# Kernel tuning notes

Hardware: AMD Instinct MI355X
Metric: run time of the kernel (lower is better)

Reference implementation:

```python
import jax, jax.numpy as jnp
import numpy as np

H, D = 20, 64  # heads, head_dim (hidden_size = 1280)


def setup_inputs() -> dict:
    key = jax.random.key(0)
    ks = jax.random.split(key, 10)
    B, S, HID, CROSS, T_TXT, T_IP = 8, 4096, 1280, 2048, 77, 4
    w = lambda k, shp: jax.random.normal(k, shp, dtype=jnp.float32) * 0.02
    return {
        "hidden_states": jax.random.normal(ks[0], (B, S, HID), dtype=jnp.float32),
        "encoder_hidden_states": jax.random.normal(ks[1], (B, T_TXT, CROSS), dtype=jnp.float32),
        "ip_hidden_states": jax.random.normal(ks[2], (B, T_IP, CROSS), dtype=jnp.float32),
        "Wq": w(ks[3], (HID, HID)),
        "Wk": w(ks[4], (CROSS, HID)),
        "Wv": w(ks[5], (CROSS, HID)),
        "Wk_ip": w(ks[6], (CROSS, HID)),
        "Wv_ip": w(ks[7], (CROSS, HID)),
        "Wo": w(ks[8], (HID, HID)),
        "bo": jnp.zeros((HID,), dtype=jnp.float32),
    }


def _attend(q, kv_in, Wk, Wv):
    # q: [B,S,H,D]; kv_in: [B,T,cross]
    B, T = kv_in.shape[0], kv_in.shape[1]
    k = (kv_in @ Wk).reshape(B, T, H, D)
    v = (kv_in @ Wv).reshape(B, T, H, D)
    scale = 1.0 / jnp.sqrt(jnp.asarray(D, q.dtype))
    scores = jnp.einsum("bqhd,bkhd->bhqk", q, k) * scale
    probs = jax.nn.softmax(scores, axis=-1)
    out = jnp.einsum("bhqk,bkhd->bqhd", probs, v)
    return out.reshape(B, q.shape[1], H * D)


def reference(hidden_states, encoder_hidden_states, ip_hidden_states,
              Wq, Wk, Wv, Wk_ip, Wv_ip, Wo, bo):
    B, S, _ = hidden_states.shape
    q = (hidden_states @ Wq).reshape(B, S, H, D)
    # text cross-attention branch
    out = _attend(q, encoder_hidden_states, Wk, Wv)
    # IP-adapter branch (single adapter, scale=1.0, no mask)
    ip_scale = 1.0
    out = out + ip_scale * _attend(q, ip_hidden_states, Wk_ip, Wv_ip)
    # output projection (dropout is identity at inference)
    return out @ Wo + bo
```

## Files before the change

kernel.cpp:

```cpp
#include <hip/hip_runtime.h>

using u16 = unsigned short;
using u32 = unsigned int;
typedef __bf16 bf16x8 __attribute__((ext_vector_type(8)));
typedef float f32x4 __attribute__((ext_vector_type(4)));
typedef float f32x16 __attribute__((ext_vector_type(16)));

__device__ __forceinline__ u16 f2bf(float f) {
  u32 u = __float_as_uint(f);
  u += 0x7FFFu + ((u >> 16) & 1u);
  return (u16)(u >> 16);
}

__device__ __forceinline__ u32 cvtpk(float a, float b) {
  u32 r;
  asm("v_cvt_pk_bf16_f32 %0, %1, %2" : "=v"(r) : "v"(a), "v"(b));
  return r;
}

__device__ __forceinline__ void gload16(const u16* g, u16* l) {
  __builtin_amdgcn_global_load_lds((const __attribute__((address_space(1))) void*)g,
                                   (__attribute__((address_space(3))) void*)l, 16, 0, 0);
}

__global__ void prep_all(const float* __restrict__ enc, const float* __restrict__ ip,
                         u16* __restrict__ a_all,
                         const float* __restrict__ Wk, const float* __restrict__ Wv,
                         const float* __restrict__ Wkip, const float* __restrict__ Wvip,
                         u16* __restrict__ kvw,
                         const float* __restrict__ Wq, const float* __restrict__ Wo,
                         u16* __restrict__ wq_t, u16* __restrict__ wo_t) {
  const int bid = blockIdx.x;
  const int tid = threadIdx.x;
  if (bid < 1536) {
    const int i = bid * 256 + tid;
    const int row = i >> 9;
    const int c4 = i & 511;
    ushort4 o = {0, 0, 0, 0};
    const float4* src = nullptr;
    if (row < 616) src = (const float4*)enc + (size_t)row * 512 + c4;
    else if (row >= 640 && row < 672) src = (const float4*)ip + (size_t)(row - 640) * 512 + c4;
    if (src) {
      const float4 v = *src;
      o.x = f2bf(v.x); o.y = f2bf(v.y); o.z = f2bf(v.z); o.w = f2bf(v.w);
    }
    ((ushort4*)a_all)[i] = o;
    return;
  }
  __shared__ float tile[32][33];
  const int x = tid & 31, y = tid >> 5;
  const float* in;
  u16* out;
  int K, N, n0, k0;
  if (bid < 11776) {
    const int f = bid - 1536;
    const int z = f / 2560, rem = f % 2560;
    in = (z == 0) ? Wk : (z == 1) ? Wv : (z == 2) ? Wkip : Wvip;
    out = kvw + (size_t)z * 1280 * 2048;
    K = 2048; N = 1280;
    n0 = (rem % 40) << 5; k0 = (rem / 40) << 5;
  } else {
    const int f = bid - 11776;
    const int z = f / 1600, rem = f % 1600;
    in = z ? Wo : Wq;
    out = z ? wo_t : wq_t;
    K = 1280; N = 1280;
    n0 = (rem % 40) << 5; k0 = (rem / 40) << 5;
  }
#pragma unroll
  for (int i = 0; i < 32; i += 8)
    tile[y + i][x] = in[(size_t)(k0 + y + i) * N + n0 + x];
  __syncthreads();
#pragma unroll
  for (int i = 0; i < 32; i += 8)
    out[(size_t)(n0 + y + i) * K + k0 + x] = f2bf(tile[x][y + i]);
}

#define MFMA16(a, b, c) __builtin_amdgcn_mfma_f32_16x16x32_bf16(a, b, c, 0, 0, 0)
#define MFMA32(a, b, c) __builtin_amdgcn_mfma_f32_32x32x16_bf16(a, b, c, 0, 0, 0)

template <int MODE, int CONV>
__global__ __launch_bounds__(512, 2) void gemm256(
    const u16* __restrict__ A, const u16* __restrict__ Bt,
    u16* __restrict__ Cb, const u16* __restrict__ kvcP, const u16* __restrict__ vtP,
    const float* __restrict__ convSrc, u16* __restrict__ convDst,
    int M, int N, int K) {
  const int tid = threadIdx.x;

  if (CONV) {
    if (blockIdx.x >= 60) {
      const float4* src = (const float4*)convSrc;
      ushort4* dst = (ushort4*)convDst;
      const long base = (long)(blockIdx.x - 60) * 4096 + tid;
#pragma unroll
      for (int k = 0; k < 8; ++k) {
        const float4 v = src[base + k * 512];
        ushort4 o;
        o.x = f2bf(v.x); o.y = f2bf(v.y); o.z = f2bf(v.z); o.w = f2bf(v.w);
        dst[base + k * 512] = o;
      }
      return;
    }
  }

  __shared__ __align__(16) u16 smem[67584];
  u16* As = smem;
  u16* Bs = smem + 32768;

  const int w = tid >> 6, lane = tid & 63;
  const int lo = lane & 15, hi = lane >> 4;
  const int wm = w >> 2, wn = w & 3;

  const int nbn = N >> 8;
  int wg = blockIdx.x;
  if (!CONV) {
    const int nwg = gridDim.x;
    const int q = nwg >> 3, r = nwg & 7;
    const int xcd = wg & 7, l = wg >> 3;
    wg = (xcd < r ? xcd * (q + 1) : r * (q + 1) + (xcd - r) * q) + l;
  }
  const int bm = wg / nbn, bn = wg % nbn;
  const int m0 = bm << 8, n0 = bn << 8;
  const int NT = K >> 6;

  const int sr = lane >> 3;
  const int sc8 = ((lane & 7) ^ sr) << 3;
  const u16* pA[2];
  const u16* pB[2];
#pragma unroll
  for (int i = 0; i < 2; ++i) {
    const int rr = (i * 8 + w) * 8 + sr;
    pA[i] = A + (size_t)(m0 + rr) * K + sc8;
    pB[i] = Bt + (size_t)(n0 + rr) * K + sc8;
  }
  const int ch0 = w * 512, ch1 = (8 + w) * 512;

#define STAGE_A(h, tt)                                                     \
  {                                                                        \
    const int ttc = ((tt) < NT) ? (tt) : (NT - 1);                         \
    u16* d = As + ((((tt)&1) * 2 + (h)) << 13);                            \
    const size_t off = (size_t)(h)*128 * K + (size_t)ttc * 64;             \
    gload16(pA[0] + off, d + ch0);                                         \
    gload16(pA[1] + off, d + ch1);                                         \
  }
#define STAGE_B(h, tt)                                                     \
  {                                                                        \
    const int ttc = ((tt) < NT) ? (tt) : (NT - 1);                         \
    u16* d = Bs + ((((tt)&1) * 2 + (h)) << 13);                            \
    const size_t off = (size_t)(h)*128 * K + (size_t)ttc * 64;             \
    gload16(pB[0] + off, d + ch0);                                         \
    gload16(pB[1] + off, d + ch1);                                         \
  }

  const int low0 = (lo << 7) | ((hi ^ (lo & 7)) << 4);
  const int low1 = (lo << 7) | (((4 | hi) ^ (lo & 7)) << 4);

  f32x4 acc[8][4];
#pragma unroll
  for (int i = 0; i < 8; ++i)
#pragma unroll
    for (int j = 0; j < 4; ++j) acc[i][j] = (f32x4){0.f, 0.f, 0.f, 0.f};

  STAGE_B(0, 0); STAGE_B(1, 0);
  STAGE_A(0, 0); STAGE_A(1, 0);
  STAGE_B(0, 1); STAGE_B(1, 1);

  const char* aSm = (const char*)As;
  const char* bSm = (const char*)Bs;

  for (int t = 0; t < NT; ++t) {
    const int p = t & 1;
    const int aBase = (p * 2 + wm) << 14;
    const int bBase = ((p * 2 + (wn >> 1)) << 14) + ((wn & 1) << 13);

    asm volatile("s_waitcnt vmcnt(4)" ::: "memory");
    asm volatile("s_barrier" ::: "memory");

    bf16x8 a0[4][2], a1[4][2], b0[2][2], b1[2][2];
#pragma unroll
    for (int mf = 0; mf < 4; ++mf) {
      a0[mf][0] = *(const bf16x8*)(aSm + aBase + (mf << 11) + low0);
      a0[mf][1] = *(const bf16x8*)(aSm + aBase + (mf << 11) + low1);
    }
#pragma unroll
    for (int nf = 0; nf < 2; ++nf) {
      b0[nf][0] = *(const bf16x8*)(bSm + bBase + (nf << 11) + low0);
      b0[nf][1] = *(const bf16x8*)(bSm + bBase + (nf << 11) + low1);
    }
    STAGE_A(0, t + 1);
    __builtin_amdgcn_s_setprio(1);
#pragma unroll
    for (int mf = 0; mf < 4; ++mf)
#pragma unroll
      for (int nf = 0; nf < 2; ++nf) {
        acc[mf][nf] = MFMA16(a0[mf][0], b0[nf][0], acc[mf][nf]);
        acc[mf][nf] = MFMA16(a0[mf][1], b0[nf][1], acc[mf][nf]);
      }
    __builtin_amdgcn_s_setprio(0);

#pragma unroll
    for (int nf = 0; nf < 2; ++nf) {
      b1[nf][0] = *(const bf16x8*)(bSm + bBase + (1 << 12) + (nf << 11) + low0);
      b1[nf][1] = *(const bf16x8*)(bSm + bBase + (1 << 12) + (nf << 11) + low1);
    }
    STAGE_A(1, t + 1);
    __builtin_amdgcn_s_setprio(1);
#pragma unroll
    for (int mf = 0; mf < 4; ++mf)
#pragma unroll
      for (int nf = 0; nf < 2; ++nf) {
        acc[mf][2 + nf] = MFMA16(a0[mf][0], b1[nf][0], acc[mf][2 + nf]);
        acc[mf][2 + nf] = MFMA16(a0[mf][1], b1[nf][1], acc[mf][2 + nf]);
      }
    __builtin_amdgcn_s_setprio(0);
    asm volatile("s_barrier" ::: "memory");

#pragma unroll
    for (int mf = 0; mf < 4; ++mf) {
      a1[mf][0] = *(const bf16x8*)(aSm + aBase + (1 << 13) + (mf << 11) + low0);
      a1[mf][1] = *(const bf16x8*)(aSm + aBase + (1 << 13) + (mf << 11) + low1);
    }
    STAGE_B(0, t + 2);
    __builtin_amdgcn_s_setprio(1);
#pragma unroll
    for (int mf = 0; mf < 4; ++mf)
#pragma unroll
      for (int nf = 0; nf < 2; ++nf) {
        acc[4 + mf][nf] = MFMA16(a1[mf][0], b0[nf][0], acc[4 + mf][nf]);
        acc[4 + mf][nf] = MFMA16(a1[mf][1], b0[nf][1], acc[4 + mf][nf]);
      }
    __builtin_amdgcn_s_setprio(0);

    STAGE_B(1, t + 2);
    __builtin_amdgcn_s_setprio(1);
#pragma unroll
    for (int mf = 0; mf < 4; ++mf)
#pragma unroll
      for (int nf = 0; nf < 2; ++nf) {
        acc[4 + mf][2 + nf] = MFMA16(a1[mf][0], b1[nf][0], acc[4 + mf][2 + nf]);
        acc[4 + mf][2 + nf] = MFMA16(a1[mf][1], b1[nf][1], acc[4 + mf][2 + nf]);
      }
    __builtin_amdgcn_s_setprio(0);
  }

  if (MODE != 2) {
#pragma unroll
    for (int g = 0; g < 2; ++g)
#pragma unroll
      for (int mf = 0; mf < 4; ++mf)
#pragma unroll
        for (int ng = 0; ng < 2; ++ng)
#pragma unroll
          for (int nfi = 0; nfi < 2; ++nfi) {
            const f32x4 v = acc[g * 4 + mf][ng * 2 + nfi];
            const int row0 = m0 + wm * 128 + g * 64 + mf * 16 + hi * 4;
            const int col = n0 + wn * 64 + ng * 32 + nfi * 16 + lo;
#pragma unroll
            for (int r = 0; r < 4; ++r)
              Cb[(size_t)(row0 + r) * N + col] = f2bf(v[r]);
          }
  } else {
    const int l31 = lane & 31, hi5 = lane >> 5;
    const int h = bn * 4 + wn;
    const int b = m0 >> 12;

    bf16x8 kreg[3][4];
#pragma unroll
    for (int kf = 0; kf < 3; ++kf) {
      const int key = kf * 32 + l31;
      const u16* kp;
      if (key < 77) kp = kvcP + (size_t)(b * 77 + key) * 5120 + h * 64 + hi5 * 8;
      else if (key >= 80 && key < 84)
        kp = kvcP + (size_t)(640 + b * 4 + key - 80) * 5120 + 2560 + h * 64 + hi5 * 8;
      else kp = kvcP + h * 64 + hi5 * 8;
#pragma unroll
      for (int dc = 0; dc < 4; ++dc) kreg[kf][dc] = *(const bf16x8*)(kp + dc * 16);
    }

    asm volatile("s_waitcnt vmcnt(0)" ::: "memory");
    __builtin_amdgcn_s_barrier();

    u16* qlds = smem + w * 8448;
#pragma unroll
    for (int g = 0; g < 2; ++g)
#pragma unroll
      for (int mf = 0; mf < 4; ++mf)
#pragma unroll
        for (int ng = 0; ng < 2; ++ng)
#pragma unroll
          for (int nfi = 0; nfi < 2; ++nfi) {
            const f32x4 v = acc[g * 4 + mf][ng * 2 + nfi];
            const int qrow = g * 64 + mf * 16 + hi * 4;
            const int d = ng * 32 + nfi * 16 + lo;
#pragma unroll
            for (int r = 0; r < 4; ++r) qlds[(qrow + r) * 66 + d] = f2bf(v[r]);
          }

    const u16* vbase = vtP + ((size_t)(b * 20 + h) * 64) * 96 + hi5 * 8;
    const int rowB = m0 + wm * 128;

#pragma unroll
    for (int pass = 0; pass < 2; ++pass) {
      bf16x8 qf0[4], qf1[4];
#pragma unroll
      for (int dc = 0; dc < 4; ++dc) {
        qf0[dc] = *(const bf16x8*)&qlds[(pass * 64 + l31) * 66 + dc * 16 + hi5 * 8];
        qf1[dc] = *(const bf16x8*)&qlds[(pass * 64 + 32 + l31) * 66 + dc * 16 + hi5 * 8];
      }

      f32x16 s0[3], s1[3];
#pragma unroll
      for (int kf = 0; kf < 3; ++kf)
#pragma unroll
        for (int r = 0; r < 16; ++r) { s0[kf][r] = 0.f; s1[kf][r] = 0.f; }

#pragma unroll
      for (int kf = 0; kf < 3; ++kf)
#pragma unroll
        for (int dc = 0; dc < 4; ++dc) {
          s0[kf] = MFMA32(kreg[kf][dc], qf0[dc], s0[kf]);
          s1[kf] = MFMA32(kreg[kf][dc], qf1[dc], s1[kf]);
        }

      float st0 = 0.f, si0 = 0.f, st1 = 0.f, si1 = 0.f;
#pragma unroll
      for (int kf = 0; kf < 3; ++kf)
#pragma unroll
        for (int r = 0; r < 16; ++r) {
          const int krem = (r & 3) + 8 * (r >> 2);
          const int k = kf * 32 + krem + 4 * hi5;
          const bool vtx = k < 77;
          const bool vip = (k >= 80) & (k < 84);
          const float e0 = (vtx | vip) ? __expf(s0[kf][r] * 0.125f) : 0.f;
          const float e1 = (vtx | vip) ? __expf(s1[kf][r] * 0.125f) : 0.f;
          s0[kf][r] = e0; s1[kf][r] = e1;
          st0 += vtx ? e0 : 0.f; si0 += vip ? e0 : 0.f;
          st1 += vtx ? e1 : 0.f; si1 += vip ? e1 : 0.f;
        }
      st0 += __shfl_xor(st0, 32); si0 += __shfl_xor(si0, 32);
      st1 += __shfl_xor(st1, 32); si1 += __shfl_xor(si1, 32);
      const float rt0 = __fdividef(1.f, st0), ri0 = __fdividef(1.f, si0);
      const float rt1 = __fdividef(1.f, st1), ri1 = __fdividef(1.f, si1);
#pragma unroll
      for (int kf = 0; kf < 3; ++kf)
#pragma unroll
        for (int r = 0; r < 16; ++r) {
          const int krem = (r & 3) + 8 * (r >> 2);
          const int k = kf * 32 + krem + 4 * hi5;
          const bool vip = (k >= 80) & (k < 84);
          s0[kf][r] *= vip ? ri0 : rt0;
          s1[kf][r] *= vip ? ri1 : rt1;
        }

#define PV_STORE(sA, qoff)                                                  \
      {                                                                     \
        f32x16 pacc[2];                                                     \
        _Pragma("unroll") for (int nf = 0; nf < 2; ++nf)                    \
        _Pragma("unroll") for (int r = 0; r < 16; ++r) pacc[nf][r] = 0.f;   \
        _Pragma("unroll") for (int ks = 0; ks < 6; ++ks) {                  \
          const int kf = ks >> 1;                                           \
          const int rb = (ks & 1) * 8;                                      \
          const u32 lo01 = cvtpk(sA[kf][rb + 0], sA[kf][rb + 1]);           \
          const u32 lo23 = cvtpk(sA[kf][rb + 2], sA[kf][rb + 3]);           \
          const u32 hi01 = cvtpk(sA[kf][rb + 4], sA[kf][rb + 5]);           \
          const u32 hi23 = cvtpk(sA[kf][rb + 6], sA[kf][rb + 7]);           \
          const u32 plo01 = __shfl_xor(lo01, 32);                           \
          const u32 plo23 = __shfl_xor(lo23, 32);                           \
          const u32 phi01 = __shfl_xor(hi01, 32);                           \
          const u32 phi23 = __shfl_xor(hi23, 32);                           \
          union { u32 u[4]; bf16x8 v; } pu;                                 \
          pu.u[0] = hi5 ? phi01 : lo01;                                     \
          pu.u[1] = hi5 ? phi23 : lo23;                                     \
          pu.u[2] = hi5 ? hi01 : plo01;                                     \
          pu.u[3] = hi5 ? hi23 : plo23;                                     \
          _Pragma("unroll") for (int nf = 0; nf < 2; ++nf) {                \
            const bf16x8 vb = *(const bf16x8*)(vbase +                      \
                (size_t)(nf * 32 + l31) * 96 + ks * 16);                    \
            pacc[nf] = MFMA32(pu.v, vb, pacc[nf]);                          \
          }                                                                 \
        }                                                                   \
        _Pragma("unroll") for (int nf = 0; nf < 2; ++nf)                    \
        _Pragma("unroll") for (int r = 0; r < 16; ++r) {                    \
          const int row = rowB + pass * 64 + (qoff) +                       \
                          (r & 3) + 8 * (r >> 2) + 4 * hi5;                 \
          Cb[(size_t)row * 1280 + h * 64 + nf * 32 + l31] =                 \
              f2bf(pacc[nf][r]);                                            \
        }                                                                   \
      }

      PV_STORE(s0, 0)
      PV_STORE(s1, 32)
#undef PV_STORE
    }
  }
#undef STAGE_A
#undef STAGE_B
}

__global__ __launch_bounds__(256, 2) void gemm128(
    const u16* __restrict__ A, const u16* __restrict__ Bt,
    float* __restrict__ Cf, const float* __restrict__ bias,
    int M, int N, int K) {
  __shared__ __align__(16) u16 smem[32768];
  const int tid = threadIdx.x;
  const int w = tid >> 6, lane = tid & 63;
  const int lo = lane & 15, hi = lane >> 4;
  const int wm = w >> 1, wn = w & 1;

  const int nbn = N >> 7;
  int wg = blockIdx.x;
  {
    const int nwg = gridDim.x;
    const int q = nwg >> 3, r = nwg & 7;
    const int xcd = wg & 7, l = wg >> 3;
    wg = (xcd < r ? xcd * (q + 1) : r * (q + 1) + (xcd - r) * q) + l;
  }
  const int bm = wg / nbn, bn = wg % nbn;
  const int m0 = bm << 7, n0 = bn << 7;
  const int NT = K >> 6;

  const int sr = lane >> 3;
  const int sc8 = ((lane & 7) ^ sr) << 3;
  const u16 *pA[4], *pB[4];
#pragma unroll
  for (int j = 0; j < 4; ++j) {
    const int rr = (w + j * 4) * 8 + sr;
    pA[j] = A + (size_t)(m0 + rr) * K + sc8;
    pB[j] = Bt + (size_t)(n0 + rr) * K + sc8;
  }

#define STG128(tt)                                                         \
  {                                                                        \
    const int ttc = ((tt) < NT) ? (tt) : (NT - 1);                         \
    const int bofs = (((tt)&1) << 13);          \
    const size_t off = (size_t)ttc * 64;                                   \
    _Pragma("unroll") for (int j = 0; j < 4; ++j) {                        \
      gload16(pA[j] + off, smem + bofs + (w + j * 4) * 512);               \
      gload16(pB[j] + off, smem + 16384 + bofs + (w + j * 4) * 512);       \
    }                                                                      \
  }

  const int low0 = (lo << 7) | ((hi ^ (lo & 7)) << 4);
  const int low1 = (lo << 7) | (((4 | hi) ^ (lo & 7)) << 4);
  const char* aSm = (const char*)smem;
  const char* bSm = (const char*)(smem + 16384);

  f32x4 acc[4][4];
#pragma unroll
  for (int i = 0; i < 4; ++i)
#pragma unroll
    for (int j = 0; j < 4; ++j) acc[i][j] = (f32x4){0.f, 0.f, 0.f, 0.f};

  STG128(0); STG128(1);

  for (int t = 0; t < NT; ++t) {
    const int aBase = ((t & 1) << 14) + (wm << 13);
    const int bBase = ((t & 1) << 14) + (wn << 13);

    asm volatile("s_waitcnt vmcnt(8)" ::: "memory");
    asm volatile("s_barrier" ::: "memory");

    bf16x8 a[4][2], b[4][2];
#pragma unroll
    for (int mf = 0; mf < 4; ++mf) {
      a[mf][0] = *(const bf16x8*)(aSm + aBase + (mf << 11) + low0);
      a[mf][1] = *(const bf16x8*)(aSm + aBase + (mf << 11) + low1);
    }
#pragma unroll
    for (int nf = 0; nf < 4; ++nf) {
      b[nf][0] = *(const bf16x8*)(bSm + bBase + (nf << 11) + low0);
      b[nf][1] = *(const bf16x8*)(bSm + bBase + (nf << 11) + low1);
    }
    asm volatile("s_waitcnt lgkmcnt(0)" ::: "memory");
    __builtin_amdgcn_sched_barrier(0);
    asm volatile("s_barrier" ::: "memory");
    STG128(t + 2);
    __builtin_amdgcn_s_setprio(1);
#pragma unroll
    for (int mf = 0; mf < 4; ++mf)
#pragma unroll
      for (int nf = 0; nf < 4; ++nf) {
        acc[mf][nf] = MFMA16(a[mf][0], b[nf][0], acc[mf][nf]);
        acc[mf][nf] = MFMA16(a[mf][1], b[nf][1], acc[mf][nf]);
      }
    __builtin_amdgcn_s_setprio(0);
  }

#pragma unroll
  for (int mf = 0; mf < 4; ++mf)
#pragma unroll
    for (int nf = 0; nf < 4; ++nf) {
      const int row0 = m0 + wm * 64 + mf * 16 + hi * 4;
      const int col = n0 + wn * 64 + nf * 16 + lo;
      const float bb = bias[col];
#pragma unroll
      for (int r = 0; r < 4; ++r)
        Cf[(size_t)(row0 + r) * N + col] = acc[mf][nf][r] + bb;
    }
#undef STG128
}

__global__ __launch_bounds__(256) void build_vt(const u16* __restrict__ kvc,
                                                u16* __restrict__ vt) {
  __shared__ u16 Ls[96][72];
  const int tid = threadIdx.x;
  const int h = blockIdx.x % 20, b = blockIdx.x / 20;
  for (int idx = tid; idx < 96 * 8; idx += 256) {
    const int row = idx >> 3, c8 = (idx & 7) << 3;
    uint4 val = make_uint4(0, 0, 0, 0);
    if (row < 77)
      val = *(const uint4*)(kvc + (size_t)(b * 77 + row) * 5120 + 1280 + h * 64 + c8);
    else if (row >= 80 && row < 84)
      val = *(const uint4*)(kvc + (size_t)(640 + b * 4 + row - 80) * 5120 + 3840 + h * 64 + c8);
    *(uint4*)&Ls[row][c8] = val;
  }
  __syncthreads();
  u16* dst = vt + (size_t)blockIdx.x * 64 * 96;
  for (int idx = tid; idx < 768; idx += 256) {
    const int d = idx / 12, c = (idx % 12) * 8;
    u16 tmp[8];
#pragma unroll
    for (int j = 0; j < 8; ++j) tmp[j] = Ls[c + j][d];
    *(uint4*)(dst + d * 96 + c) = *(const uint4*)tmp;
  }
}

extern "C" void kernel_launch(void* const* d_in, const int* in_sizes, int n_in,
                              void* d_out, int out_size, void* d_ws, size_t ws_size,
                              hipStream_t stream) {
  (void)in_sizes; (void)n_in; (void)out_size; (void)ws_size;
  const float* hs   = (const float*)d_in[0];
  const float* enc  = (const float*)d_in[1];
  const float* ip   = (const float*)d_in[2];
  const float* Wq   = (const float*)d_in[3];
  const float* Wk   = (const float*)d_in[4];
  const float* Wv   = (const float*)d_in[5];
  const float* Wkip = (const float*)d_in[6];
  const float* Wvip = (const float*)d_in[7];
  const float* Wo   = (const float*)d_in[8];
  const float* bo   = (const float*)d_in[9];
  float* out = (float*)d_out;

  u16* wq_t  = (u16*)d_out;
  u16* hs_bf = (u16*)d_out + 41943040;

  char* ws = (char*)d_ws;
  u16* kvc   = (u16*)(ws);
  u16* wo_t  = (u16*)(ws + 15728640);
  u16* vt    = (u16*)(ws + 19005440);
  u16* attn  = (u16*)(ws + 20971520);
  u16* kvw   = (u16*)(ws + 20971520 + 3276800);
  u16* a_all = (u16*)(ws + 20971520 + 24248320);

  prep_all<<<14976, 256, 0, stream>>>(enc, ip, a_all, Wk, Wv, Wkip, Wvip, kvw,
                                      Wq, Wo, wq_t, wo_t);

  gemm256<0, 1><<<2620, 512, 0, stream>>>(a_all, kvw, kvc, nullptr, nullptr,
                                          hs, hs_bf, 768, 5120, 2048);
  build_vt<<<160, 256, 0, stream>>>(kvc, vt);

  gemm256<2, 0><<<640, 512, 0, stream>>>(hs_bf, wq_t, attn, kvc, vt,
                                         nullptr, nullptr, 32768, 1280, 1280);

  gemm128<<<2560, 256, 0, stream>>>(attn, wo_t, out, bo, 32768, 1280, 1280);
}
```

Baseline: 334.9 us.

## Move fused Q-projection attention epilogue from 256-tile to 128-tile GEMM

The Q projection with its fused cross-attention and IP-attention epilogue now runs on the 128x128-tile, 256-thread GEMM kernel with 2560 workgroups, instead of the 256x256-tile, 512-thread kernel with 640 workgroups. The 256 kernel is specialised to the KV projection plus conversion, which drops its XCD remap. The aim is to fix under-filled waves and improve occupancy and load balance across CUs for the 32768x1280 GEMM. The cost is lower tile reuse, so more global and LDS traffic per FLOP, and each workgroup now reloads K fragments for fewer query rows.

Result: slower. 347.3 us (+3.7%).

```diff
diff --git a/kernel.cpp b/kernel.cpp
--- a/kernel.cpp
+++ b/kernel.cpp
@@ -79,31 +79,27 @@
 #define MFMA16(a, b, c) __builtin_amdgcn_mfma_f32_16x16x32_bf16(a, b, c, 0, 0, 0)
 #define MFMA32(a, b, c) __builtin_amdgcn_mfma_f32_32x32x16_bf16(a, b, c, 0, 0, 0)
 
-template <int MODE, int CONV>
-__global__ __launch_bounds__(512, 2) void gemm256(
-    const u16* __restrict__ A, const u16* __restrict__ Bt,
-    u16* __restrict__ Cb, const u16* __restrict__ kvcP, const u16* __restrict__ vtP,
+__global__ __launch_bounds__(512, 2) void gemm256kv(
+    const u16* __restrict__ A, const u16* __restrict__ Bt, u16* __restrict__ Cb,
     const float* __restrict__ convSrc, u16* __restrict__ convDst,
     int M, int N, int K) {
   const int tid = threadIdx.x;
 
-  if (CONV) {
-    if (blockIdx.x >= 60) {
-      const float4* src = (const float4*)convSrc;
-      ushort4* dst = (ushort4*)convDst;
-      const long base = (long)(blockIdx.x - 60) * 4096 + tid;
-#pragma unroll
-      for (int k = 0; k < 8; ++k) {
-        const float4 v = src[base + k * 512];
-        ushort4 o;
-        o.x = f2bf(v.x); o.y = f2bf(v.y); o.z = f2bf(v.z); o.w = f2bf(v.w);
-        dst[base + k * 512] = o;
-      }
-      return;
-    }
-  }
-
-  __shared__ __align__(16) u16 smem[67584];
+  if (blockIdx.x >= 60) {
+    const float4* src = (const float4*)convSrc;
+    ushort4* dst = (ushort4*)convDst;
+    const long base = (long)(blockIdx.x - 60) * 4096 + tid;
+#pragma unroll
+    for (int k = 0; k < 8; ++k) {
+      const float4 v = src[base + k * 512];
+      ushort4 o;
+      o.x = f2bf(v.x); o.y = f2bf(v.y); o.z = f2bf(v.z); o.w = f2bf(v.w);
+      dst[base + k * 512] = o;
+    }
+    return;
+  }
+
+  __shared__ __align__(16) u16 smem[65536];
   u16* As = smem;
   u16* Bs = smem + 32768;
 
@@ -112,13 +108,7 @@
   const int wm = w >> 2, wn = w & 3;
 
   const int nbn = N >> 8;
-  int wg = blockIdx.x;
-  if (!CONV) {
-    const int nwg = gridDim.x;
-    const int q = nwg >> 3, r = nwg & 7;
-    const int xcd = wg & 7, l = wg >> 3;
-    wg = (xcd < r ? xcd * (q + 1) : r * (q + 1) + (xcd - r) * q) + l;
-  }
+  const int wg = blockIdx.x;
   const int bm = wg / nbn, bn = wg % nbn;
   const int m0 = bm << 8, n0 = bn << 8;
   const int NT = K >> 6;
@@ -243,163 +233,30 @@
     __builtin_amdgcn_s_setprio(0);
   }
 
-  if (MODE != 2) {
-#pragma unroll
-    for (int g = 0; g < 2; ++g)
-#pragma unroll
-      for (int mf = 0; mf < 4; ++mf)
-#pragma unroll
-        for (int ng = 0; ng < 2; ++ng)
-#pragma unroll
-          for (int nfi = 0; nfi < 2; ++nfi) {
-            const f32x4 v = acc[g * 4 + mf][ng * 2 + nfi];
-            const int row0 = m0 + wm * 128 + g * 64 + mf * 16 + hi * 4;
-            const int col = n0 + wn * 64 + ng * 32 + nfi * 16 + lo;
-#pragma unroll
-            for (int r = 0; r < 4; ++r)
-              Cb[(size_t)(row0 + r) * N + col] = f2bf(v[r]);
-          }
-  } else {
-    const int l31 = lane & 31, hi5 = lane >> 5;
-    const int h = bn * 4 + wn;
-    const int b = m0 >> 12;
-
-    bf16x8 kreg[3][4];
-#pragma unroll
-    for (int kf = 0; kf < 3; ++kf) {
-      const int key = kf * 32 + l31;
-      const u16* kp;
-      if (key < 77) kp = kvcP + (size_t)(b * 77 + key) * 5120 + h * 64 + hi5 * 8;
-      else if (key >= 80 && key < 84)
-        kp = kvcP + (size_t)(640 + b * 4 + key - 80) * 5120 + 2560 + h * 64 + hi5 * 8;
-      else kp = kvcP + h * 64 + hi5 * 8;
-#pragma unroll
-      for (int dc = 0; dc < 4; ++dc) kreg[kf][dc] = *(const bf16x8*)(kp + dc * 16);
-    }
-
-    asm volatile("s_waitcnt vmcnt(0)" ::: "memory");
-    __builtin_amdgcn_s_barrier();
-
-    u16* qlds = smem + w * 8448;
-#pragma unroll
-    for (int g = 0; g < 2; ++g)
-#pragma unroll
-      for (int mf = 0; mf < 4; ++mf)
-#pragma unroll
-        for (int ng = 0; ng < 2; ++ng)
-#pragma unroll
-          for (int nfi = 0; nfi < 2; ++nfi) {
-            const f32x4 v = acc[g * 4 + mf][ng * 2 + nfi];
-            const int qrow = g * 64 + mf * 16 + hi * 4;
-            const int d = ng * 32 + nfi * 16 + lo;
-#pragma unroll
-            for (int r = 0; r < 4; ++r) qlds[(qrow + r) * 66 + d] = f2bf(v[r]);
-          }
-
-    const u16* vbase = vtP + ((size_t)(b * 20 + h) * 64) * 96 + hi5 * 8;
-    const int rowB = m0 + wm * 128;
-
-#pragma unroll
-    for (int pass = 0; pass < 2; ++pass) {
-      bf16x8 qf0[4], qf1[4];
-#pragma unroll
-      for (int dc = 0; dc < 4; ++dc) {
-        qf0[dc] = *(const bf16x8*)&qlds[(pass * 64 + l31) * 66 + dc * 16 + hi5 * 8];
-        qf1[dc] = *(const bf16x8*)&qlds[(pass * 64 + 32 + l31) * 66 + dc * 16 + hi5 * 8];
-      }
-
-      f32x16 s0[3], s1[3];
-#pragma unroll
-      for (int kf = 0; kf < 3; ++kf)
-#pragma unroll
-        for (int r = 0; r < 16; ++r) { s0[kf][r] = 0.f; s1[kf][r] = 0.f; }
-
-#pragma unroll
-      for (int kf = 0; kf < 3; ++kf)
-#pragma unroll
-        for (int dc = 0; dc < 4; ++dc) {
-          s0[kf] = MFMA32(kreg[kf][dc], qf0[dc], s0[kf]);
-          s1[kf] = MFMA32(kreg[kf][dc], qf1[dc], s1[kf]);
+#pragma unroll
+  for (int g = 0; g < 2; ++g)
+#pragma unroll
+    for (int mf = 0; mf < 4; ++mf)
+#pragma unroll
+      for (int ng = 0; ng < 2; ++ng)
+#pragma unroll
+        for (int nfi = 0; nfi < 2; ++nfi) {
+          const f32x4 v = acc[g * 4 + mf][ng * 2 + nfi];
+          const int row0 = m0 + wm * 128 + g * 64 + mf * 16 + hi * 4;
+          const int col = n0 + wn * 64 + ng * 32 + nfi * 16 + lo;
+#pragma unroll
+          for (int r = 0; r < 4; ++r)
+            Cb[(size_t)(row0 + r) * N + col] = f2bf(v[r]);
         }
-
-      float st0 = 0.f, si0 = 0.f, st1 = 0.f, si1 = 0.f;
-#pragma unroll
-      for (int kf = 0; kf < 3; ++kf)
-#pragma unroll
-        for (int r = 0; r < 16; ++r) {
-          const int krem = (r & 3) + 8 * (r >> 2);
-          const int k = kf * 32 + krem + 4 * hi5;
-          const bool vtx = k < 77;
-          const bool vip = (k >= 80) & (k < 84);
-          const float e0 = (vtx | vip) ? __expf(s0[kf][r] * 0.125f) : 0.f;
-          const float e1 = (vtx | vip) ? __expf(s1[kf][r] * 0.125f) : 0.f;
-          s0[kf][r] = e0; s1[kf][r] = e1;
-          st0 += vtx ? e0 : 0.f; si0 += vip ? e0 : 0.f;
-          st1 += vtx ? e1 : 0.f; si1 += vip ? e1 : 0.f;
-        }
-      st0 += __shfl_xor(st0, 32); si0 += __shfl_xor(si0, 32);
-      st1 += __shfl_xor(st1, 32); si1 += __shfl_xor(si1, 32);
-      const float rt0 = __fdividef(1.f, st0), ri0 = __fdividef(1.f, si0);
-      const float rt1 = __fdividef(1.f, st1), ri1 = __fdividef(1.f, si1);
-#pragma unroll
-      for (int kf = 0; kf < 3; ++kf)
-#pragma unroll
-        for (int r = 0; r < 16; ++r) {
-          const int krem = (r & 3) + 8 * (r >> 2);
-          const int k = kf * 32 + krem + 4 * hi5;
-          const bool vip = (k >= 80) & (k < 84);
-          s0[kf][r] *= vip ? ri0 : rt0;
-          s1[kf][r] *= vip ? ri1 : rt1;
-        }
-
-#define PV_STORE(sA, qoff)                                                  \
-      {                                                                     \
-        f32x16 pacc[2];                                                     \
-        _Pragma("unroll") for (int nf = 0; nf < 2; ++nf)                    \
-        _Pragma("unroll") for (int r = 0; r < 16; ++r) pacc[nf][r] = 0.f;   \
-        _Pragma("unroll") for (int ks = 0; ks < 6; ++ks) {                  \
-          const int kf = ks >> 1;                                           \
-          const int rb = (ks & 1) * 8;                                      \
-          const u32 lo01 = cvtpk(sA[kf][rb + 0], sA[kf][rb + 1]);           \
-          const u32 lo23 = cvtpk(sA[kf][rb + 2], sA[kf][rb + 3]);           \
-          const u32 hi01 = cvtpk(sA[kf][rb + 4], sA[kf][rb + 5]);           \
-          const u32 hi23 = cvtpk(sA[kf][rb + 6], sA[kf][rb + 7]);           \
-          const u32 plo01 = __shfl_xor(lo01, 32);                           \
-          const u32 plo23 = __shfl_xor(lo23, 32);                           \
-          const u32 phi01 = __shfl_xor(hi01, 32);                           \
-          const u32 phi23 = __shfl_xor(hi23, 32);                           \
-          union { u32 u[4]; bf16x8 v; } pu;                                 \
-          pu.u[0] = hi5 ? phi01 : lo01;                                     \
-          pu.u[1] = hi5 ? phi23 : lo23;                                     \
-          pu.u[2] = hi5 ? hi01 : plo01;                                     \
-          pu.u[3] = hi5 ? hi23 : plo23;                                     \
-          _Pragma("unroll") for (int nf = 0; nf < 2; ++nf) {                \
-            const bf16x8 vb = *(const bf16x8*)(vbase +                      \
-                (size_t)(nf * 32 + l31) * 96 + ks * 16);                    \
-            pacc[nf] = MFMA32(pu.v, vb, pacc[nf]);                          \
-          }                                                                 \
-        }                                                                   \
-        _Pragma("unroll") for (int nf = 0; nf < 2; ++nf)                    \
-        _Pragma("unroll") for (int r = 0; r < 16; ++r) {                    \
-          const int row = rowB + pass * 64 + (qoff) +                       \
-                          (r & 3) + 8 * (r >> 2) + 4 * hi5;                 \
-          Cb[(size_t)row * 1280 + h * 64 + nf * 32 + l31] =                 \
-              f2bf(pacc[nf][r]);                                            \
-        }                                                                   \
-      }
-
-      PV_STORE(s0, 0)
-      PV_STORE(s1, 32)
-#undef PV_STORE
-    }
-  }
 #undef STAGE_A
 #undef STAGE_B
 }
 
+template <int MODE>
 __global__ __launch_bounds__(256, 2) void gemm128(
     const u16* __restrict__ A, const u16* __restrict__ Bt,
-    float* __restrict__ Cf, const float* __restrict__ bias,
+    u16* __restrict__ Cb, float* __restrict__ Cf, const float* __restrict__ bias,
+    const u16* __restrict__ kvcP, const u16* __restrict__ vtP,
     int M, int N, int K) {
   __shared__ __align__(16) u16 smem[32768];
   const int tid = threadIdx.x;
@@ -486,17 +343,143 @@
     __builtin_amdgcn_s_setprio(0);
   }
 
-#pragma unroll
-  for (int mf = 0; mf < 4; ++mf)
-#pragma unroll
-    for (int nf = 0; nf < 4; ++nf) {
-      const int row0 = m0 + wm * 64 + mf * 16 + hi * 4;
-      const int col = n0 + wn * 64 + nf * 16 + lo;
-      const float bb = bias[col];
-#pragma unroll
-      for (int r = 0; r < 4; ++r)
-        Cf[(size_t)(row0 + r) * N + col] = acc[mf][nf][r] + bb;
-    }
+  if (MODE == 1) {
+#pragma unroll
+    for (int mf = 0; mf < 4; ++mf)
+#pragma unroll
+      for (int nf = 0; nf < 4; ++nf) {
+        const int row0 = m0 + wm * 64 + mf * 16 + hi * 4;
+        const int col = n0 + wn * 64 + nf * 16 + lo;
+        const float bb = bias[col];
+#pragma unroll
+        for (int r = 0; r < 4; ++r)
+          Cf[(size_t)(row0 + r) * N + col] = acc[mf][nf][r] + bb;
+      }
+  } else {
+    const int l31 = lane & 31, hi5 = lane >> 5;
+    const int h = bn * 2 + wn;
+    const int b = m0 >> 12;
+
+    bf16x8 kreg[3][4];
+#pragma unroll
+    for (int kf = 0; kf < 3; ++kf) {
+      const int key = kf * 32 + l31;
+      const u16* kp;
+      if (key < 77) kp = kvcP + (size_t)(b * 77 + key) * 5120 + h * 64 + hi5 * 8;
+      else if (key >= 80 && key < 84)
+        kp = kvcP + (size_t)(640 + b * 4 + key - 80) * 5120 + 2560 + h * 64 + hi5 * 8;
+      else kp = kvcP + h * 64 + hi5 * 8;
+#pragma unroll
+      for (int dc = 0; dc < 4; ++dc) kreg[kf][dc] = *(const bf16x8*)(kp + dc * 16);
+    }
+
+    asm volatile("s_waitcnt vmcnt(0)" ::: "memory");
+    __builtin_amdgcn_s_barrier();
+
+    u16* qlds = smem + w * 4224;
+#pragma unroll
+    for (int mf = 0; mf < 4; ++mf)
+#pragma unroll
+      for (int nf = 0; nf < 4; ++nf) {
+        const f32x4 v = acc[mf][nf];
+        const int qrow = mf * 16 + hi * 4;
+        const int d = nf * 16 + lo;
+#pragma unroll
+        for (int r = 0; r < 4; ++r) qlds[(qrow + r) * 66 + d] = f2bf(v[r]);
+      }
+
+    bf16x8 qf0[4], qf1[4];
+#pragma unroll
+    for (int dc = 0; dc < 4; ++dc) {
+      qf0[dc] = *(const bf16x8*)&qlds[(l31)*66 + dc * 16 + hi5 * 8];
+      qf1[dc] = *(const bf16x8*)&qlds[(32 + l31) * 66 + dc * 16 + hi5 * 8];
+    }
+
+    f32x16 s0[3], s1[3];
+#pragma unroll
+    for (int kf = 0; kf < 3; ++kf)
+#pragma unroll
+      for (int r = 0; r < 16; ++r) { s0[kf][r] = 0.f; s1[kf][r] = 0.f; }
+
+#pragma unroll
+    for (int kf = 0; kf < 3; ++kf)
+#pragma unroll
+      for (int dc = 0; dc < 4; ++dc) {
+        s0[kf] = MFMA32(kreg[kf][dc], qf0[dc], s0[kf]);
+        s1[kf] = MFMA32(kreg[kf][dc], qf1[dc], s1[kf]);
+      }
+
+    float st0 = 0.f, si0 = 0.f, st1 = 0.f, si1 = 0.f;
+#pragma unroll
+    for (int kf = 0; kf < 3; ++kf)
+#pragma unroll
+      for (int r = 0; r < 16; ++r) {
+        const int krem = (r & 3) + 8 * (r >> 2);
+        const int k = kf * 32 + krem + 4 * hi5;
+        const bool vtx = k < 77;
+        const bool vip = (k >= 80) & (k < 84);
+        const float e0 = (vtx | vip) ? __expf(s0[kf][r] * 0.125f) : 0.f;
+        const float e1 = (vtx | vip) ? __expf(s1[kf][r] * 0.125f) : 0.f;
+        s0[kf][r] = e0; s1[kf][r] = e1;
+        st0 += vtx ? e0 : 0.f; si0 += vip ? e0 : 0.f;
+        st1 += vtx ? e1 : 0.f; si1 += vip ? e1 : 0.f;
+      }
+    st0 += __shfl_xor(st0, 32); si0 += __shfl_xor(si0, 32);
+    st1 += __shfl_xor(st1, 32); si1 += __shfl_xor(si1, 32);
+    const float rt0 = __fdividef(1.f, st0), ri0 = __fdividef(1.f, si0);
+    const float rt1 = __fdividef(1.f, st1), ri1 = __fdividef(1.f, si1);
+#pragma unroll
+    for (int kf = 0; kf < 3; ++kf)
+#pragma unroll
+      for (int r = 0; r < 16; ++r) {
+        const int krem = (r & 3) + 8 * (r >> 2);
+        const int k = kf * 32 + krem + 4 * hi5;
+        const bool vip = (k >= 80) & (k < 84);
+        s0[kf][r] *= vip ? ri0 : rt0;
+        s1[kf][r] *= vip ? ri1 : rt1;
+      }
+
+    const u16* vbase = vtP + ((size_t)(b * 20 + h) * 64) * 96 + hi5 * 8;
+    const int rowB = m0 + wm * 64;
+
+#define PV_STORE(sA, qoff)                                                  \
+    {                                                                       \
+      f32x16 pacc[2];                                                       \
+      _Pragma("unroll") for (int nf = 0; nf < 2; ++nf)                      \
+      _Pragma("unroll") for (int r = 0; r < 16; ++r) pacc[nf][r] = 0.f;     \
+      _Pragma("unroll") for (int ks = 0; ks < 6; ++ks) {                    \
+        const int kf = ks >> 1;                                             \
+        const int rb = (ks & 1) * 8;                                        \
+        const u32 lo01 = cvtpk(sA[kf][rb + 0], sA[kf][rb + 1]);             \
+        const u32 lo23 = cvtpk(sA[kf][rb + 2], sA[kf][rb + 3]);             \
+        const u32 hi01 = cvtpk(sA[kf][rb + 4], sA[kf][rb + 5]);             \
+        const u32 hi23 = cvtpk(sA[kf][rb + 6], sA[kf][rb + 7]);             \
+        const u32 plo01 = __shfl_xor(lo01, 32);                             \
+        const u32 plo23 = __shfl_xor(lo23, 32);                             \
+        const u32 phi01 = __shfl_xor(hi01, 32);                             \
+        const u32 phi23 = __shfl_xor(hi23, 32);                             \
+        union { u32 u[4]; bf16x8 v; } pu;                                   \
+        pu.u[0] = hi5 ? phi01 : lo01;                                       \
+        pu.u[1] = hi5 ? phi23 : lo23;                                       \
+        pu.u[2] = hi5 ? hi01 : plo01;                                       \
+        pu.u[3] = hi5 ? hi23 : plo23;                                       \
+        _Pragma("unroll") for (int nf = 0; nf < 2; ++nf) {                  \
+          const bf16x8 vb = *(const bf16x8*)(vbase +                        \
+              (size_t)(nf * 32 + l31) * 96 + ks * 16);                      \
+          pacc[nf] = MFMA32(pu.v, vb, pacc[nf]);                            \
+        }                                                                   \
+      }                                                                     \
+      _Pragma("unroll") for (int nf = 0; nf < 2; ++nf)                      \
+      _Pragma("unroll") for (int r = 0; r < 16; ++r) {                      \
+        const int row = rowB + (qoff) + (r & 3) + 8 * (r >> 2) + 4 * hi5;   \
+        Cb[(size_t)row * 1280 + h * 64 + nf * 32 + l31] = f2bf(pacc[nf][r]);\
+      }                                                                     \
+    }
+
+    PV_STORE(s0, 0)
+    PV_STORE(s1, 32)
+#undef PV_STORE
+  }
 #undef STG128
 }
 
@@ -555,12 +538,12 @@
   prep_all<<<14976, 256, 0, stream>>>(enc, ip, a_all, Wk, Wv, Wkip, Wvip, kvw,
                                       Wq, Wo, wq_t, wo_t);
 
-  gemm256<0, 1><<<2620, 512, 0, stream>>>(a_all, kvw, kvc, nullptr, nullptr,
-                                          hs, hs_bf, 768, 5120, 2048);
+  gemm256kv<<<2620, 512, 0, stream>>>(a_all, kvw, kvc, hs, hs_bf, 768, 5120, 2048);
   build_vt<<<160, 256, 0, stream>>>(kvc, vt);
 
-  gemm256<2, 0><<<640, 512, 0, stream>>>(hs_bf, wq_t, attn, kvc, vt,
-                                         nullptr, nullptr, 32768, 1280, 1280);
-
-  gemm128<<<2560, 256, 0, stream>>>(attn, wo_t, out, bo, 32768, 1280, 1280);
-}
+  gemm128<2><<<2560, 256, 0, stream>>>(hs_bf, wq_t, attn, nullptr, nullptr,
+                                       kvc, vt, 32768, 1280, 1280);
+
+  gemm128<1><<<2560, 256, 0, stream>>>(attn, wo_t, nullptr, out, bo,
+                                       nullptr, nullptr, 32768, 1280, 1280);
+}
```
